# Kernel optimization log

Hardware: AMD Instinct MI355X
Metric: run time of the kernel (lower is better)

The kernel has to match this reference:

```python
import jax, jax.numpy as jnp
import numpy as np

DIM = 1024
NUM_HEADS = 16
HEAD_DIM = DIM // NUM_HEADS
SCALE = HEAD_DIM ** -0.5


def setup_inputs() -> dict:
    key = jax.random.key(0)
    k_x, k_wqkv, k_bqkv, k_wp, k_bp = jax.random.split(key, 5)
    B, C, D = 4, 1024, DIM
    x = jax.random.normal(k_x, (B, C, D), dtype=jnp.float32)
    # nn.Linear stores weight as (out, in); we keep (in, out) for x @ W
    w_qkv = jax.random.normal(k_wqkv, (D, 3 * D), dtype=jnp.float32) * (D ** -0.5)
    b_qkv = jax.random.normal(k_bqkv, (3 * D,), dtype=jnp.float32) * 0.02
    w_proj = jax.random.normal(k_wp, (D, D), dtype=jnp.float32) * (D ** -0.5)
    b_proj = jax.random.normal(k_bp, (D,), dtype=jnp.float32) * 0.02
    return {"x": x, "w_qkv": w_qkv, "b_qkv": b_qkv, "w_proj": w_proj, "b_proj": b_proj}


def reference(x, w_qkv, b_qkv, w_proj, b_proj):
    B, C, D = x.shape
    H, Hd = NUM_HEADS, HEAD_DIM
    qkv = x @ w_qkv + b_qkv                       # (B, C, 3D)
    qkv = qkv.reshape(B, C, 3, H, Hd)
    q = qkv[:, :, 0].transpose(0, 2, 1, 3)        # (B, H, C, Hd)
    k = qkv[:, :, 1].transpose(0, 2, 1, 3)
    v = qkv[:, :, 2].transpose(0, 2, 1, 3)
    attn = jnp.einsum('bhqd,bhkd->bhqk', q, k) * SCALE
    attn = jax.nn.softmax(attn, axis=-1)
    out = jnp.einsum('bhqk,bhkd->bhqd', attn, v)  # (B, H, C, Hd)
    out = out.transpose(0, 2, 1, 3).reshape(B, C, D)
    return out @ w_proj + b_proj
```

## Files before the change

kernel.cpp:

```cpp
#include <hip/hip_runtime.h>
#include <cstdint>

#define BB 4
#define CC 1024
#define DD 1024
#define HH 16
#define HD 64
#define NH3 3072

typedef __attribute__((ext_vector_type(8))) short short8;
typedef __attribute__((ext_vector_type(4))) float f32x4;

#define MFMA16(a, b, c) __builtin_amdgcn_mfma_f32_16x16x32_bf16(a, b, c, 0, 0, 0)

__device__ __forceinline__ void glds16(const void* g, void* l) {
    __builtin_amdgcn_global_load_lds(
        (const __attribute__((address_space(1))) void*)g,
        (__attribute__((address_space(3))) void*)l, 16, 0, 0);
}

__device__ __forceinline__ ushort f2bf(float f) {
    union { float f; uint32_t u; } v; v.f = f;
    uint32_t r = v.u + 0x7FFF + ((v.u >> 16) & 1);
    return (ushort)(r >> 16);
}

__device__ __forceinline__ uint32_t pack2bf(float a, float b) {
    return (uint32_t)f2bf(a) | ((uint32_t)f2bf(b) << 16);
}

__global__ __launch_bounds__(256)
void prep_kernel(const float* __restrict__ x, ushort* __restrict__ xbf,
                 const float* __restrict__ wqkv, ushort* __restrict__ wqkvT,
                 const float* __restrict__ wprj, ushort* __restrict__ wprjT)
{
    __shared__ float Ts[64 * 65];
    const int blk = blockIdx.x;
    const int t = threadIdx.x;

    if (blk < 4096) {
        int i = blk * 256 + t;
        float4 v = ((const float4*)x)[i];
        ushort4 o;
        o.x = f2bf(v.x); o.y = f2bf(v.y); o.z = f2bf(v.z); o.w = f2bf(v.w);
        ((ushort4*)xbf)[i] = o;
        return;
    }

    const float* in; ushort* outp; int K, N, n0, k0;
    if (blk < 4864) {
        int bx = blk - 4096;
        in = wqkv; outp = wqkvT; K = DD; N = NH3;
        n0 = (bx % 48) * 64; k0 = (bx / 48) * 64;
    } else {
        int bx = blk - 4864;
        in = wprj; outp = wprjT; K = DD; N = DD;
        n0 = (bx % 16) * 64; k0 = (bx / 16) * 64;
    }
    #pragma unroll
    for (int i = 0; i < 16; ++i) {
        int idx = t + i * 256;
        int r = idx >> 6, c = idx & 63;
        Ts[r * 65 + c] = in[(size_t)(k0 + r) * N + n0 + c];
    }
    __syncthreads();
    #pragma unroll
    for (int i = 0; i < 16; ++i) {
        int idx = t + i * 256;
        int rr = idx >> 6, cc = idx & 63;
        outp[(size_t)(n0 + rr) * K + k0 + cc] = f2bf(Ts[cc * 65 + rr]);
    }
}

template<int MODE>
__global__ __launch_bounds__(256)
void gemm_bt(const ushort* __restrict__ A, const ushort* __restrict__ Bt,
             const float* __restrict__ bias, float* __restrict__ Cf,
             ushort* __restrict__ qb, ushort* __restrict__ kb, ushort* __restrict__ vtb,
             int M, int N, int K)
{
    __shared__ ushort As[2][128 * 32];
    __shared__ ushort Bs[2][128 * 32];

    const int tid = threadIdx.x;
    const int wid = tid >> 6, lane = tid & 63;
    const int quad = lane >> 4, l15 = lane & 15;
    const int m0 = blockIdx.y * 128, n0 = blockIdx.x * 128;
    const int wm = (wid >> 1) * 64, wn = (wid & 1) * 64;

    const int sr = lane >> 2;
    const int sc = lane & 3;

    const int r0 = wid * 32 + sr;
    const int cg0 = sc ^ ((r0 >> 1) & 3);
    const int cg1 = sc ^ (((r0 + 16) >> 1) & 3);
    const ushort* Ar0 = A  + (size_t)(m0 + r0) * K + cg0 * 8;
    const ushort* Ar1 = A  + (size_t)(m0 + r0 + 16) * K + cg1 * 8;
    const ushort* Br0 = Bt + (size_t)(n0 + r0) * K + cg0 * 8;
    const ushort* Br1 = Bt + (size_t)(n0 + r0 + 16) * K + cg1 * 8;

    f32x4 acc[4][4];
    #pragma unroll
    for (int i = 0; i < 4; ++i)
        #pragma unroll
        for (int j = 0; j < 4; ++j) acc[i][j] = (f32x4)(0.0f);

    {
        glds16(Ar0, &As[0][(wid * 32) * 32]);
        glds16(Br0, &Bs[0][(wid * 32) * 32]);
        glds16(Ar1, &As[0][(wid * 32 + 16) * 32]);
        glds16(Br1, &Bs[0][(wid * 32 + 16) * 32]);
    }

    int buf = 0;
    for (int k0 = 0; k0 < K; k0 += 32) {
        __syncthreads();
        if (k0 + 32 < K) {
            const int kn = k0 + 32;
            glds16(Ar0 + kn, &As[buf ^ 1][(wid * 32) * 32]);
            glds16(Br0 + kn, &Bs[buf ^ 1][(wid * 32) * 32]);
            glds16(Ar1 + kn, &As[buf ^ 1][(wid * 32 + 16) * 32]);
            glds16(Br1 + kn, &Bs[buf ^ 1][(wid * 32 + 16) * 32]);
        }

        short8 af[4], bf[4];
        #pragma unroll
        for (int i = 0; i < 4; ++i) {
            int row = wm + i * 16 + l15;
            af[i] = *(const short8*)(&As[buf][row * 32 + (quad ^ ((row >> 1) & 3)) * 8]);
            int col = wn + i * 16 + l15;
            bf[i] = *(const short8*)(&Bs[buf][col * 32 + (quad ^ ((col >> 1) & 3)) * 8]);
        }
        #pragma unroll
        for (int i = 0; i < 4; ++i)
            #pragma unroll
            for (int j = 0; j < 4; ++j)
                acc[i][j] = MFMA16(af[i], bf[j], acc[i][j]);
        buf ^= 1;
    }

    if (MODE == 0) {
        #pragma unroll
        for (int i = 0; i < 4; ++i) {
            int row = m0 + wm + i * 16 + quad * 4;
            #pragma unroll
            for (int j = 0; j < 4; ++j) {
                int col = n0 + wn + j * 16 + l15;
                float bv = bias[col];
                #pragma unroll
                for (int r = 0; r < 4; ++r)
                    Cf[(size_t)(row + r) * N + col] = acc[i][j][r] + bv;
            }
        }
    } else {
        #pragma unroll
        for (int j = 0; j < 4; ++j) {
            int n = n0 + wn + j * 16 + l15;
            int three = n >> 10;
            int h = (n >> 6) & 15;
            int hd = n & 63;
            float scale = (three == 0) ? 0.1803368801f : 1.0f;
            float bv = bias[n];
            #pragma unroll
            for (int i = 0; i < 4; ++i) {
                int row = m0 + wm + i * 16 + quad * 4;
                #pragma unroll
                for (int r = 0; r < 4; ++r) {
                    int m = row + r;
                    int b = m >> 10, c = m & 1023;
                    ushort val = f2bf((acc[i][j][r] + bv) * scale);
                    if (three == 0)
                        qb[((size_t)((b * HH + h) * CC) + c) * HD + hd] = val;
                    else if (three == 1)
                        kb[((size_t)((b * HH + h) * CC) + c) * HD + hd] = val;
                    else
                        vtb[((size_t)((b * HH + h) * HD) + hd) * CC + c] = val;
                }
            }
        }
    }
}

__global__ __launch_bounds__(256)
void attn_mfma3(const ushort* __restrict__ qb, const ushort* __restrict__ kb,
                const ushort* __restrict__ vt, ushort* __restrict__ attnb)
{
    __shared__ ushort Ks[2][64 * 64];
    __shared__ ushort Vs[2][64 * 64];
    __shared__ ushort Ps[128 * 72];

    const int tid = threadIdx.x;
    const int wid = tid >> 6, lane = tid & 63;
    const int quad = lane >> 4, l15 = lane & 15;
    const int qt = blockIdx.x, bh = blockIdx.y;
    const int q0 = qt * 128;
    const int b = bh >> 4, h = bh & 15;

    const ushort* Qp  = qb + ((size_t)bh * CC + q0) * HD;
    const ushort* Kp  = kb + (size_t)bh * CC * HD;
    const ushort* Vtp = vt + (size_t)bh * HD * CC;

    const int sr = lane >> 3;
    const int sc = lane & 7;

    short8 qf[2][2];
    #pragma unroll
    for (int q2 = 0; q2 < 2; ++q2) {
        int row = wid * 32 + q2 * 16 + l15;
        #pragma unroll
        for (int s = 0; s < 2; ++s)
            qf[q2][s] = *(const short8*)(Qp + (size_t)row * HD + (s * 4 + quad) * 8);
    }

    const int kr = wid * 16 + sr;
    const int cgA = sc ^ (kr & 7);
    const int cgB = sc ^ ((kr + 8) & 7);
    const ushort* Kr0 = Kp  + (size_t)kr * HD + cgA * 8;
    const ushort* Kr1 = Kp  + (size_t)(kr + 8) * HD + cgB * 8;
    const ushort* Vr0 = Vtp + (size_t)kr * CC + cgA * 8;
    const ushort* Vr1 = Vtp + (size_t)(kr + 8) * CC + cgB * 8;

    glds16(Kr0, &Ks[0][(wid * 16) * 64]);
    glds16(Vr0, &Vs[0][(wid * 16) * 64]);
    glds16(Kr1, &Ks[0][(wid * 16 + 8) * 64]);
    glds16(Vr1, &Vs[0][(wid * 16 + 8) * 64]);

    f32x4 oacc[2][4];
    #pragma unroll
    for (int q2 = 0; q2 < 2; ++q2)
        #pragma unroll
        for (int hb = 0; hb < 4; ++hb) oacc[q2][hb] = (f32x4)(0.0f);
    float lsum[2] = {0.0f, 0.0f};

    int buf = 0;
    for (int kt = 0; kt < 16; ++kt) {
        __syncthreads();
        if (kt < 15) {
            const int koff = (kt + 1) * 64;
            glds16(Kr0 + (size_t)koff * HD, &Ks[buf ^ 1][(wid * 16) * 64]);
            glds16(Vr0 + koff,              &Vs[buf ^ 1][(wid * 16) * 64]);
            glds16(Kr1 + (size_t)koff * HD, &Ks[buf ^ 1][(wid * 16 + 8) * 64]);
            glds16(Vr1 + koff,              &Vs[buf ^ 1][(wid * 16 + 8) * 64]);
        }

        #pragma unroll
        for (int kb2 = 0; kb2 < 4; ++kb2) {
            int krow = kb2 * 16 + l15;
            short8 kf0 = *(const short8*)(&Ks[buf][krow * 64 + ((quad ^ (krow & 7)) * 8)]);
            short8 kf1 = *(const short8*)(&Ks[buf][krow * 64 + (((4 + quad) ^ (krow & 7)) * 8)]);
            #pragma unroll
            for (int q2 = 0; q2 < 2; ++q2) {
                f32x4 st = (f32x4)(0.0f);
                st = MFMA16(kf0, qf[q2][0], st);
                st = MFMA16(kf1, qf[q2][1], st);
                float p0 = exp2f(st[0]);
                float p1 = exp2f(st[1]);
                float p2 = exp2f(st[2]);
                float p3 = exp2f(st[3]);
                lsum[q2] += (p0 + p1) + (p2 + p3);
                int row = wid * 32 + q2 * 16 + l15;
                *(uint2*)(Ps + row * 72 + kb2 * 16 + quad * 4) =
                    make_uint2(pack2bf(p0, p1), pack2bf(p2, p3));
            }
        }

        short8 vf[4][2];
        #pragma unroll
        for (int hb = 0; hb < 4; ++hb) {
            int hr = hb * 16 + l15;
            vf[hb][0] = *(const short8*)(&Vs[buf][hr * 64 + ((quad ^ (hr & 7)) * 8)]);
            vf[hb][1] = *(const short8*)(&Vs[buf][hr * 64 + (((4 + quad) ^ (hr & 7)) * 8)]);
        }
        #pragma unroll
        for (int q2 = 0; q2 < 2; ++q2) {
            int row = wid * 32 + q2 * 16 + l15;
            short8 pf0 = *(const short8*)(Ps + row * 72 + quad * 8);
            short8 pf1 = *(const short8*)(Ps + row * 72 + 32 + quad * 8);
            #pragma unroll
            for (int hb = 0; hb < 4; ++hb) {
                oacc[q2][hb] = MFMA16(pf0, vf[hb][0], oacc[q2][hb]);
                oacc[q2][hb] = MFMA16(pf1, vf[hb][1], oacc[q2][hb]);
            }
        }
        buf ^= 1;
    }

    #pragma unroll
    for (int q2 = 0; q2 < 2; ++q2) {
        lsum[q2] += __shfl_xor(lsum[q2], 16);
        lsum[q2] += __shfl_xor(lsum[q2], 32);
    }

    #pragma unroll
    for (int q2 = 0; q2 < 2; ++q2) {
        #pragma unroll
        for (int r = 0; r < 4; ++r) {
            float inv = 1.0f / __shfl(lsum[q2], (lane & 48) | (quad * 4 + r));
            int c = q0 + wid * 32 + q2 * 16 + quad * 4 + r;
            #pragma unroll
            for (int hb = 0; hb < 4; ++hb) {
                int d = h * 64 + hb * 16 + l15;
                attnb[((size_t)(b * CC + c)) * DD + d] = f2bf(oacc[q2][hb][r] * inv);
            }
        }
    }
}

extern "C" void kernel_launch(void* const* d_in, const int* in_sizes, int n_in,
                              void* d_out, int out_size, void* d_ws, size_t ws_size,
                              hipStream_t stream)
{
    (void)in_sizes; (void)n_in; (void)out_size; (void)ws_size;
    const float* x      = (const float*)d_in[0];
    const float* w_qkv  = (const float*)d_in[1];
    const float* b_qkv  = (const float*)d_in[2];
    const float* w_proj = (const float*)d_in[3];
    const float* b_proj = (const float*)d_in[4];
    float* out = (float*)d_out;

    ushort* p = (ushort*)d_ws;
    ushort* xbf   = p;  p += (size_t)4 * 1024 * 1024;
    ushort* wqkvT = p;  p += (size_t)3 * 1024 * 1024;
    ushort* wprjT = p;  p += (size_t)1 * 1024 * 1024;
    ushort* qbuf  = p;  p += (size_t)4 * 1024 * 1024;
    ushort* kbuf  = p;  p += (size_t)4 * 1024 * 1024;
    ushort* vtb   = p;  p += (size_t)4 * 1024 * 1024;
    ushort* attnb = p;  p += (size_t)4 * 1024 * 1024;

    prep_kernel<<<5120, 256, 0, stream>>>(x, xbf, w_qkv, wqkvT, w_proj, wprjT);

    gemm_bt<1><<<dim3(NH3 / 128, (BB * CC) / 128), 256, 0, stream>>>(
        xbf, wqkvT, b_qkv, nullptr, qbuf, kbuf, vtb, BB * CC, NH3, DD);

    attn_mfma3<<<dim3(8, 64), 256, 0, stream>>>(qbuf, kbuf, vtb, attnb);

    gemm_bt<0><<<dim3(DD / 128, (BB * CC) / 128), 256, 0, stream>>>(
        attnb, wprjT, b_proj, out, nullptr, nullptr, nullptr, BB * CC, DD, DD);
}
```

Measured before the change: 191.8 us.

## Software-pipeline attention PV with previous tile and double-buffer P

The attention kernel is restructured so that each iteration computes the P·V product for the previous key tile while computing QK^T and exp for the current tile. P now has two shared-memory buffers, and the V loads are issued one step later to match. This aims to remove the barrier-separated dependency between softmax and PV so that MFMA and exp work can overlap. It also switches to the hardware exp2 intrinsic and a perm-based bf16 packing, at the cost of more LDS and a fully unrolled loop with higher register pressure.

```diff
diff --git a/kernel.cpp b/kernel.cpp
--- a/kernel.cpp
+++ b/kernel.cpp
@@ -12,6 +12,7 @@
 typedef __attribute__((ext_vector_type(4))) float f32x4;
 
 #define MFMA16(a, b, c) __builtin_amdgcn_mfma_f32_16x16x32_bf16(a, b, c, 0, 0, 0)
+#define EXP2 __builtin_amdgcn_exp2f
 
 __device__ __forceinline__ void glds16(const void* g, void* l) {
     __builtin_amdgcn_global_load_lds(
@@ -26,7 +27,10 @@
 }
 
 __device__ __forceinline__ uint32_t pack2bf(float a, float b) {
-    return (uint32_t)f2bf(a) | ((uint32_t)f2bf(b) << 16);
+    uint32_t ua = __float_as_uint(a), ub = __float_as_uint(b);
+    ua += 0x7FFF + ((ua >> 16) & 1);
+    ub += 0x7FFF + ((ub >> 16) & 1);
+    return __builtin_amdgcn_perm(ua, ub, 0x03020706);
 }
 
 __global__ __launch_bounds__(256)
@@ -105,12 +109,10 @@
         #pragma unroll
         for (int j = 0; j < 4; ++j) acc[i][j] = (f32x4)(0.0f);
 
-    {
-        glds16(Ar0, &As[0][(wid * 32) * 32]);
-        glds16(Br0, &Bs[0][(wid * 32) * 32]);
-        glds16(Ar1, &As[0][(wid * 32 + 16) * 32]);
-        glds16(Br1, &Bs[0][(wid * 32 + 16) * 32]);
-    }
+    glds16(Ar0, &As[0][(wid * 32) * 32]);
+    glds16(Br0, &Bs[0][(wid * 32) * 32]);
+    glds16(Ar1, &As[0][(wid * 32 + 16) * 32]);
+    glds16(Br1, &Bs[0][(wid * 32 + 16) * 32]);
 
     int buf = 0;
     for (int k0 = 0; k0 < K; k0 += 32) {
@@ -182,12 +184,12 @@
 }
 
 __global__ __launch_bounds__(256)
-void attn_mfma3(const ushort* __restrict__ qb, const ushort* __restrict__ kb,
+void attn_mfma4(const ushort* __restrict__ qb, const ushort* __restrict__ kb,
                 const ushort* __restrict__ vt, ushort* __restrict__ attnb)
 {
     __shared__ ushort Ks[2][64 * 64];
     __shared__ ushort Vs[2][64 * 64];
-    __shared__ ushort Ps[128 * 72];
+    __shared__ ushort Ps[2][128 * 72];
 
     const int tid = threadIdx.x;
     const int wid = tid >> 6, lane = tid & 63;
@@ -221,9 +223,7 @@
     const ushort* Vr1 = Vtp + (size_t)(kr + 8) * CC + cgB * 8;
 
     glds16(Kr0, &Ks[0][(wid * 16) * 64]);
-    glds16(Vr0, &Vs[0][(wid * 16) * 64]);
     glds16(Kr1, &Ks[0][(wid * 16 + 8) * 64]);
-    glds16(Vr1, &Vs[0][(wid * 16 + 8) * 64]);
 
     f32x4 oacc[2][4];
     #pragma unroll
@@ -232,57 +232,84 @@
         for (int hb = 0; hb < 4; ++hb) oacc[q2][hb] = (f32x4)(0.0f);
     float lsum[2] = {0.0f, 0.0f};
 
-    int buf = 0;
+    #pragma unroll
     for (int kt = 0; kt < 16; ++kt) {
+        const int cur = kt & 1, prev = (kt - 1) & 1, nxt = (kt + 1) & 1;
         __syncthreads();
         if (kt < 15) {
-            const int koff = (kt + 1) * 64;
-            glds16(Kr0 + (size_t)koff * HD, &Ks[buf ^ 1][(wid * 16) * 64]);
-            glds16(Vr0 + koff,              &Vs[buf ^ 1][(wid * 16) * 64]);
-            glds16(Kr1 + (size_t)koff * HD, &Ks[buf ^ 1][(wid * 16 + 8) * 64]);
-            glds16(Vr1 + koff,              &Vs[buf ^ 1][(wid * 16 + 8) * 64]);
+            const size_t ko = (size_t)(kt + 1) * 64 * HD;
+            glds16(Kr0 + ko, &Ks[nxt][(wid * 16) * 64]);
+            glds16(Kr1 + ko, &Ks[nxt][(wid * 16 + 8) * 64]);
+        }
+        {
+            const int vo = kt * 64;
+            glds16(Vr0 + vo, &Vs[cur][(wid * 16) * 64]);
+            glds16(Vr1 + vo, &Vs[cur][(wid * 16 + 8) * 64]);
+        }
+
+        if (kt > 0) {
+            short8 vf[4][2];
+            #pragma unroll
+            for (int hb = 0; hb < 4; ++hb) {
+                int hr = hb * 16 + l15;
+                vf[hb][0] = *(const short8*)(&Vs[prev][hr * 64 + ((quad ^ (hr & 7)) * 8)]);
+                vf[hb][1] = *(const short8*)(&Vs[prev][hr * 64 + (((4 + quad) ^ (hr & 7)) * 8)]);
+            }
+            #pragma unroll
+            for (int q2 = 0; q2 < 2; ++q2) {
+                int row = wid * 32 + q2 * 16 + l15;
+                short8 pf0 = *(const short8*)(&Ps[prev][row * 72 + quad * 8]);
+                short8 pf1 = *(const short8*)(&Ps[prev][row * 72 + 32 + quad * 8]);
+                #pragma unroll
+                for (int hb = 0; hb < 4; ++hb) {
+                    oacc[q2][hb] = MFMA16(pf0, vf[hb][0], oacc[q2][hb]);
+                    oacc[q2][hb] = MFMA16(pf1, vf[hb][1], oacc[q2][hb]);
+                }
+            }
         }
 
         #pragma unroll
         for (int kb2 = 0; kb2 < 4; ++kb2) {
             int krow = kb2 * 16 + l15;
-            short8 kf0 = *(const short8*)(&Ks[buf][krow * 64 + ((quad ^ (krow & 7)) * 8)]);
-            short8 kf1 = *(const short8*)(&Ks[buf][krow * 64 + (((4 + quad) ^ (krow & 7)) * 8)]);
+            short8 kf0 = *(const short8*)(&Ks[cur][krow * 64 + ((quad ^ (krow & 7)) * 8)]);
+            short8 kf1 = *(const short8*)(&Ks[cur][krow * 64 + (((4 + quad) ^ (krow & 7)) * 8)]);
             #pragma unroll
             for (int q2 = 0; q2 < 2; ++q2) {
                 f32x4 st = (f32x4)(0.0f);
                 st = MFMA16(kf0, qf[q2][0], st);
                 st = MFMA16(kf1, qf[q2][1], st);
-                float p0 = exp2f(st[0]);
-                float p1 = exp2f(st[1]);
-                float p2 = exp2f(st[2]);
-                float p3 = exp2f(st[3]);
+                float p0 = EXP2(st[0]);
+                float p1 = EXP2(st[1]);
+                float p2 = EXP2(st[2]);
+                float p3 = EXP2(st[3]);
                 lsum[q2] += (p0 + p1) + (p2 + p3);
                 int row = wid * 32 + q2 * 16 + l15;
-                *(uint2*)(Ps + row * 72 + kb2 * 16 + quad * 4) =
+                *(uint2*)(&Ps[cur][row * 72 + kb2 * 16 + quad * 4]) =
                     make_uint2(pack2bf(p0, p1), pack2bf(p2, p3));
             }
         }
-
+    }
+
+    __syncthreads();
+    {
         short8 vf[4][2];
         #pragma unroll
         for (int hb = 0; hb < 4; ++hb) {
             int hr = hb * 16 + l15;
-            vf[hb][0] = *(const short8*)(&Vs[buf][hr * 64 + ((quad ^ (hr & 7)) * 8)]);
-            vf[hb][1] = *(const short8*)(&Vs[buf][hr * 64 + (((4 + quad) ^ (hr & 7)) * 8)]);
+            vf[hb][0] = *(const short8*)(&Vs[1][hr * 64 + ((quad ^ (hr & 7)) * 8)]);
+            vf[hb][1] = *(const short8*)(&Vs[1][hr * 64 + (((4 + quad) ^ (hr & 7)) * 8)]);
         }
         #pragma unroll
         for (int q2 = 0; q2 < 2; ++q2) {
             int row = wid * 32 + q2 * 16 + l15;
-            short8 pf0 = *(const short8*)(Ps + row * 72 + quad * 8);
-            short8 pf1 = *(const short8*)(Ps + row * 72 + 32 + quad * 8);
+            short8 pf0 = *(const short8*)(&Ps[1][row * 72 + quad * 8]);
+            short8 pf1 = *(const short8*)(&Ps[1][row * 72 + 32 + quad * 8]);
             #pragma unroll
             for (int hb = 0; hb < 4; ++hb) {
                 oacc[q2][hb] = MFMA16(pf0, vf[hb][0], oacc[q2][hb]);
                 oacc[q2][hb] = MFMA16(pf1, vf[hb][1], oacc[q2][hb]);
             }
         }
-        buf ^= 1;
     }
 
     #pragma unroll
@@ -332,7 +359,7 @@
     gemm_bt<1><<<dim3(NH3 / 128, (BB * CC) / 128), 256, 0, stream>>>(
         xbf, wqkvT, b_qkv, nullptr, qbuf, kbuf, vtb, BB * CC, NH3, DD);
 
-    attn_mfma3<<<dim3(8, 64), 256, 0, stream>>>(qbuf, kbuf, vtb, attnb);
+    attn_mfma4<<<dim3(8, 64), 256, 0, stream>>>(qbuf, kbuf, vtb, attnb);
 
     gemm_bt<0><<<dim3(DD / 128, (BB * CC) / 128), 256, 0, stream>>>(
         attnb, wprjT, b_proj, out, nullptr, nullptr, nullptr, BB * CC, DD, DD);
```

Result: slower. 220.0 us (+14.7%).
